# Kernel optimization log

Measured on AMD Instinct MI355X. Metric: run time of the kernel, lower is better.

## Reference

```python
import jax, jax.numpy as jnp
import numpy as np

ROBOT_W = 1.0
PHASE_W = 1.0
COHER_W = 10.0
SPEED_W = 5.0
MAX_SPEED = 10.0
SMOOTH_VEL_W = 0.05
SMOOTH_ACC_W = 0.01

# illegal phase transitions {(0,2),(1,0),(2,0),(2,1)} as a 3x3 lookup table
_ILLEGAL = np.zeros((3, 3), dtype=bool)
for a, b in [(0, 2), (1, 0), (2, 0), (2, 1)]:
    _ILLEGAL[a, b] = True
ILLEGAL_TABLE = jnp.asarray(_ILLEGAL)


def setup_inputs() -> dict:
    key = jax.random.key(0)
    k1, k2, k3, k4 = jax.random.split(key, 4)
    B, T = 256, 8192
    # scale by 8 so per-frame speeds (norm of diffs of 3-vectors) exceed MAX_SPEED
    pred_robot = jax.random.normal(k1, (B, T, 12), dtype=jnp.float32) * 8.0
    gt_robot = jax.random.normal(k2, (B, T, 12), dtype=jnp.float32) * 8.0
    pred_phase = jax.random.normal(k3, (B, T, 3), dtype=jnp.float32)
    gt_phase = jax.random.randint(k4, (B, T), 0, 3, dtype=jnp.int32)
    return {"pred_robot": pred_robot, "pred_phase": pred_phase,
            "gt_robot": gt_robot, "gt_phase": gt_phase}


def _coherence_loss(phase_logits):
    # vectorized replacement for the O(B*T) Python double loop
    p = jnp.argmax(phase_logits, axis=-1)            # [B, T]
    pt, pt1 = p[:, :-1], p[:, 1:]                    # [B, T-1]
    illegal = ILLEGAL_TABLE[pt, pt1]                 # [B, T-1] bool
    # logit of the (illegal) predicted phase at t+1
    sel = jnp.take_along_axis(phase_logits[:, 1:], pt1[..., None], axis=-1)[..., 0]
    loss_sum = jnp.sum(jnp.where(illegal, sel * sel, 0.0))
    count = jnp.sum(illegal)
    return jnp.where(count > 0, loss_sum / jnp.maximum(count, 1).astype(sel.dtype), 0.0)


def _speed_loss(pred_robot):
    B, T, D = pred_robot.shape
    vel = pred_robot[:, 1:] - pred_robot[:, :-1]     # [B, T-1, 12]
    pts = vel.reshape(B, T - 1, 4, 3)
    speeds = jnp.linalg.norm(pts, axis=-1)           # [B, T-1, 4]
    pen = jax.nn.relu(speeds - MAX_SPEED)
    return SPEED_W * jnp.mean(pen * pen)


def reference(pred_robot, pred_phase, gt_robot, gt_phase):
    # MSE over robot trajectory
    robot_loss = jnp.mean((pred_robot - gt_robot) ** 2)
    # cross-entropy over 3 phase classes
    logp = jax.nn.log_softmax(pred_phase, axis=-1)   # [B, T, 3]
    nll = -jnp.take_along_axis(logp, gt_phase[..., None].astype(jnp.int32), axis=-1)[..., 0]
    phase_loss = jnp.mean(nll)
    coherence = _coherence_loss(pred_phase)
    speed_loss = _speed_loss(pred_robot)
    vel = pred_robot[:, 1:] - pred_robot[:, :-1]
    vel_loss = jnp.mean(vel * vel)
    acc = pred_robot[:, 2:] - 2.0 * pred_robot[:, 1:-1] + pred_robot[:, :-2]
    acc_loss = jnp.mean(acc * acc)
    total = (ROBOT_W * robot_loss + PHASE_W * phase_loss + COHER_W * coherence
             + speed_loss + SMOOTH_VEL_W * vel_loss + SMOOTH_ACC_W * acc_loss)
    return total
```

## Files before the change

kernel.cpp:

```cpp
#include <hip/hip_runtime.h>
#include <math.h>

#define B_DIM 256
#define T_DIM 8192
#define BLOCK 256
#define GRID  1024
#define NSLOT 256
#define ROWS_TOT (B_DIM * T_DIM)
#define NPAIR (ROWS_TOT / 2)
#define NT    (GRID * BLOCK)
#define NITER (NPAIR / NT)
#define NF4   (ROWS_TOT * 3)


__device__ __forceinline__ float pen_term(float s) {
    float d = fmaxf(sqrtf(s) - 10.0f, 0.0f);
    return d * d;
}
__device__ __forceinline__ void argmax3(float l0, float l1, float l2, int &p, float &m) {
    p = 0; m = l0;
    if (l1 > m) { m = l1; p = 1; }
    if (l2 > m) { m = l2; p = 2; }
}
__device__ __forceinline__ float nll3(float l0, float l1, float l2, int g) {
    float mx = fmaxf(l0, fmaxf(l1, l2));
    float s = __expf(l0 - mx) + __expf(l1 - mx) + __expf(l2 - mx);
    float sel = (g == 0) ? l0 : ((g == 1) ? l1 : l2);
    return mx + __logf(s) - sel;
}
__device__ __forceinline__ void sse4(const float4 &a, const float4 &g, float &s) {
    float d;
    d = a.x - g.x; s = fmaf(d, d, s);  d = a.y - g.y; s = fmaf(d, d, s);
    d = a.z - g.z; s = fmaf(d, d, s);  d = a.w - g.w; s = fmaf(d, d, s);
}
__device__ __forceinline__ void vel12(const float4 &p0a, const float4 &p0b, const float4 &p0c,
                                      const float4 &p1a, const float4 &p1b, const float4 &p1c,
                                      float &velsq, float &pen2) {
    float t;
    t = p1a.x - p0a.x; const float q0  = t * t;
    t = p1a.y - p0a.y; const float q1  = t * t;
    t = p1a.z - p0a.z; const float q2  = t * t;
    t = p1a.w - p0a.w; const float q3  = t * t;
    t = p1b.x - p0b.x; const float q4  = t * t;
    t = p1b.y - p0b.y; const float q5  = t * t;
    t = p1b.z - p0b.z; const float q6  = t * t;
    t = p1b.w - p0b.w; const float q7  = t * t;
    t = p1c.x - p0c.x; const float q8  = t * t;
    t = p1c.y - p0c.y; const float q9  = t * t;
    t = p1c.z - p0c.z; const float q10 = t * t;
    t = p1c.w - p0c.w; const float q11 = t * t;
    velsq += (q0 + q1 + q2 + q3) + (q4 + q5 + q6 + q7) + (q8 + q9 + q10 + q11);
    pen2  += pen_term(q0 + q1 + q2) + pen_term(q3 + q4 + q5)
           + pen_term(q6 + q7 + q8) + pen_term(q9 + q10 + q11);
}
__device__ __forceinline__ void acc4(const float4 &r0, const float4 &r1, const float4 &r2, float &accsq) {
    float a;
    a = r2.x - 2.0f * r1.x + r0.x; accsq = fmaf(a, a, accsq);
    a = r2.y - 2.0f * r1.y + r0.y; accsq = fmaf(a, a, accsq);
    a = r2.z - 2.0f * r1.z + r0.z; accsq = fmaf(a, a, accsq);
    a = r2.w - 2.0f * r1.w + r0.w; accsq = fmaf(a, a, accsq);
}

__global__ __launch_bounds__(BLOCK, 4) void combined_loss_main(
    const float4* __restrict__ pred4,
    const float*  __restrict__ ph,
    const float4* __restrict__ gt4,
    const int*    __restrict__ gt_phase,
    double* __restrict__ ws)
{
    __shared__ float s_red[4][6];
    const int tid  = threadIdx.x;
    const int blk  = blockIdx.x;
    const int gtid = blk * BLOCK + tid;

    float sse = 0.f, nllv = 0.f, csum = 0.f, ccnt = 0.f;
    float pen2 = 0.f, velsq = 0.f, accsq = 0.f;

    #pragma unroll 1
    for (int u = 0; u < NITER; ++u) {
        const int P = u * NT + gtid;
        const bool tail = ((P + 1) & 4095) == 0;
        const size_t fp = (size_t)P * 6;
        const size_t ep = tail ? fp : fp + 6;

        const float4 A0 = pred4[fp + 0], A1 = pred4[fp + 1], A2 = pred4[fp + 2];
        const float4 A3 = pred4[fp + 3], A4 = pred4[fp + 4], A5 = pred4[fp + 5];
        const float4 G0 = gt4[fp + 0],   G1 = gt4[fp + 1],   G2 = gt4[fp + 2];
        const float4 G3 = gt4[fp + 3],   G4 = gt4[fp + 4],   G5 = gt4[fp + 5];
        const float4 E0 = pred4[ep + 0], E1 = pred4[ep + 1], E2 = pred4[ep + 2];
        const float4 E3 = pred4[ep + 3], E4 = pred4[ep + 4], E5 = pred4[ep + 5];

        sse4(A0, G0, sse); sse4(A1, G1, sse); sse4(A2, G2, sse);
        sse4(A3, G3, sse); sse4(A4, G4, sse); sse4(A5, G5, sse);

        vel12(A0, A1, A2, A3, A4, A5, velsq, pen2);
        if (!tail) {
            vel12(A3, A4, A5, E0, E1, E2, velsq, pen2);
            acc4(A0, A3, E0, accsq);
            acc4(A1, A4, E1, accsq);
            acc4(A2, A5, E2, accsq);
            acc4(A3, E0, E3, accsq);
            acc4(A4, E1, E4, accsq);
            acc4(A5, E2, E5, accsq);
        }
    }

    const float2* ph2  = (const float2*)ph;
    const int2*   gtp2 = (const int2*)gt_phase;
    #pragma unroll 1
    for (int u = 0; u < NITER; ++u) {
        const int L = u * NT + gtid;
        const bool tail = ((L + 1) & 4095) == 0;
        const size_t pb = (size_t)L * 3;
        const size_t qb = tail ? pb : pb + 3;

        const float2 a  = ph2[pb + 0], b = ph2[pb + 1], c = ph2[pb + 2];
        const float2 e0 = ph2[qb + 0], e1 = ph2[qb + 1];
        const int2   gg = gtp2[L];

        nllv += nll3(a.x, a.y, b.x, gg.x);
        nllv += nll3(b.y, c.x, c.y, gg.y);

        int p0, p1, p2; float m0, m1, m2;
        argmax3(a.x,  a.y,  b.x,  p0, m0);
        argmax3(b.y,  c.x,  c.y,  p1, m1);
        argmax3(e0.x, e0.y, e1.x, p2, m2);

        const int mask0 = (p0 == 0) ? 4 : ((p0 == 1) ? 1 : 3);
        if ((mask0 >> p1) & 1) { csum += m1 * m1; ccnt += 1.f; }
        if (!tail) {
            const int mask1 = (p1 == 0) ? 4 : ((p1 == 1) ? 1 : 3);
            if ((mask1 >> p2) & 1) { csum += m2 * m2; ccnt += 1.f; }
        }
    }

    float vals[6] = { fmaf(12.0f, nllv, sse), csum, ccnt, pen2, velsq, accsq };
    #pragma unroll
    for (int off = 32; off > 0; off >>= 1) {
        #pragma unroll
        for (int q = 0; q < 6; ++q)
            vals[q] += __shfl_down(vals[q], off, 64);
    }
    const int wave = tid >> 6, lane = tid & 63;
    if (lane == 0) {
        #pragma unroll
        for (int q = 0; q < 6; ++q) s_red[wave][q] = vals[q];
    }
    __syncthreads();
    if (tid < 6) {
        const double acc = (double)s_red[0][tid] + (double)s_red[1][tid]
                         + (double)s_red[2][tid] + (double)s_red[3][tid];
        atomicAdd(&ws[(size_t)(blk & (NSLOT - 1)) * 8 + tid], acc);
    }
}

__global__ __launch_bounds__(256) void combined_loss_final(
    const double* __restrict__ ws, float* __restrict__ out)
{
    __shared__ double sred[4][6];
    const int tid = threadIdx.x;
    double v[6];
    #pragma unroll
    for (int q = 0; q < 6; ++q) v[q] = ws[(size_t)tid * 8 + q];
    #pragma unroll
    for (int off = 32; off > 0; off >>= 1) {
        #pragma unroll
        for (int q = 0; q < 6; ++q)
            v[q] += __shfl_down(v[q], off, 64);
    }
    const int wave = tid >> 6, lane = tid & 63;
    if (lane == 0) {
        #pragma unroll
        for (int q = 0; q < 6; ++q) sred[wave][q] = v[q];
    }
    __syncthreads();
    if (tid == 0) {
        double s[6];
        #pragma unroll
        for (int q = 0; q < 6; ++q)
            s[q] = sred[0][q] + sred[1][q] + sred[2][q] + sred[3][q];
        const double robot_phase = s[0] / (double)((size_t)B_DIM * T_DIM * 12);
        const double coher = (s[2] > 0.0) ? (s[1] / fmax(s[2], 1.0)) : 0.0;
        const double speed = 5.0  * (s[3] / (double)((size_t)B_DIM * (T_DIM - 1) * 4));
        const double vel   = 0.05 * (s[4] / (double)((size_t)B_DIM * (T_DIM - 1) * 12));
        const double acc   = 0.01 * (s[5] / (double)((size_t)B_DIM * (T_DIM - 2) * 12));
        out[0] = (float)(robot_phase + 10.0 * coher + speed + vel + acc);
    }
}

extern "C" void kernel_launch(void* const* d_in, const int* in_sizes, int n_in,
                              void* d_out, int out_size, void* d_ws, size_t ws_size,
                              hipStream_t stream)
{
    const float4* pred4      = (const float4*)d_in[0];
    const float*  pred_phase = (const float*)d_in[1];
    const float4* gt4        = (const float4*)d_in[2];
    const int*    gt_phase   = (const int*)d_in[3];
    double* ws  = (double*)d_ws;
    float*  out = (float*)d_out;

    hipMemsetAsync(d_ws, 0, (size_t)NSLOT * 8 * sizeof(double), stream);

    combined_loss_main<<<dim3(GRID), BLOCK, 0, stream>>>(pred4, pred_phase, gt4, gt_phase, ws);
    combined_loss_final<<<1, 256, 0, stream>>>(ws, out);
}
```

Before: 243.5 us.

## Stage row tiles into double-buffered LDS via async global-to-LDS loads

```diff
diff --git a/kernel.cpp b/kernel.cpp
--- a/kernel.cpp
+++ b/kernel.cpp
@@ -4,14 +4,66 @@
 #define B_DIM 256
 #define T_DIM 8192
 #define BLOCK 256
-#define GRID  1024
 #define NSLOT 256
 #define ROWS_TOT (B_DIM * T_DIM)
-#define NPAIR (ROWS_TOT / 2)
-#define NT    (GRID * BLOCK)
-#define NITER (NPAIR / NT)
-#define NF4   (ROWS_TOT * 3)
-
+#define NF4  (ROWS_TOT * 3)
+#define TILE_ROWS 256
+#define NTILES (ROWS_TOT / TILE_ROWS)
+#define GRID 1024
+#define TPB (NTILES / GRID)
+
+#define L_GT   768
+#define L_PHG  1536
+#define BUF_F4 1792
+
+
+__device__ __forceinline__ void dma16(const void* g, void* l) {
+    __builtin_amdgcn_global_load_lds(
+        (const __attribute__((address_space(1))) void*)g,
+        (__attribute__((address_space(3))) void*)l, 16, 0, 0);
+}
+
+__device__ __forceinline__ void stage_tile(int R, int tid, float4* buf,
+    const float4* __restrict__ pred4, const float4* __restrict__ gt4,
+    const float*  __restrict__ ph,    const int*    __restrict__ gtp)
+{
+    const char* gp = (const char*)(pred4 + (size_t)R * 3);
+    const char* gg = (const char*)(gt4   + (size_t)R * 3);
+    char* lb = (char*)buf;
+    const int o = tid * 16;
+    dma16(gp + o,        lb + o);
+    dma16(gp + 4096 + o, lb + 4096 + o);
+    dma16(gp + 8192 + o, lb + 8192 + o);
+    dma16(gg + o,        lb + 12288 + o);
+    dma16(gg + 4096 + o, lb + 16384 + o);
+    dma16(gg + 8192 + o, lb + 20480 + o);
+    const char* gm = (tid < 192)
+        ? ((const char*)(ph + (size_t)R * 3) + o)
+        : ((const char*)(gtp + R) + (o - 3072));
+    dma16(gm, lb + 24576 + o);
+}
+
+struct Bnd {
+    float4 e0a, e0b, e0c;
+    float4 e1a, e1b, e1c;
+    float  q0, q1, q2;
+};
+
+__device__ __forceinline__ void load_bnd(int R, int tid, Bnd &b,
+    const float4* __restrict__ pred4, const float* __restrict__ ph)
+{
+    if (tid >= BLOCK - 2) {
+        int r1 = R + 256, r2 = R + 257;
+        if (r1 >= ROWS_TOT) r1 = R;
+        if (r2 >= ROWS_TOT) r2 = R;
+        const float4* p1 = pred4 + (size_t)r1 * 3;
+        const float4* p2 = pred4 + (size_t)r2 * 3;
+        b.e0a = p1[0]; b.e0b = p1[1]; b.e0c = p1[2];
+        b.e1a = p2[0]; b.e1b = p2[1]; b.e1c = p2[2];
+        const float* pp = ph + (size_t)r1 * 3;
+        b.q0 = pp[0]; b.q1 = pp[1]; b.q2 = pp[2];
+    }
+}
 
 __device__ __forceinline__ float pen_term(float s) {
     float d = fmaxf(sqrtf(s) - 10.0f, 0.0f);
@@ -61,77 +113,94 @@
     a = r2.w - 2.0f * r1.w + r0.w; accsq = fmaf(a, a, accsq);
 }
 
-__global__ __launch_bounds__(BLOCK, 4) void combined_loss_main(
+__global__ __launch_bounds__(BLOCK) void combined_loss_main(
     const float4* __restrict__ pred4,
     const float*  __restrict__ ph,
     const float4* __restrict__ gt4,
     const int*    __restrict__ gt_phase,
     double* __restrict__ ws)
 {
-    __shared__ float s_red[4][6];
-    const int tid  = threadIdx.x;
-    const int blk  = blockIdx.x;
-    const int gtid = blk * BLOCK + tid;
+    __shared__ float4 lds[2][BUF_F4];
+    __shared__ float  s_red[4][6];
+
+    const int tid = threadIdx.x;
+    const int blk = blockIdx.x;
+    const int t0  = blk * TPB;
 
     float sse = 0.f, nllv = 0.f, csum = 0.f, ccnt = 0.f;
     float pen2 = 0.f, velsq = 0.f, accsq = 0.f;
 
-    #pragma unroll 1
-    for (int u = 0; u < NITER; ++u) {
-        const int P = u * NT + gtid;
-        const bool tail = ((P + 1) & 4095) == 0;
-        const size_t fp = (size_t)P * 6;
-        const size_t ep = tail ? fp : fp + 6;
-
-        const float4 A0 = pred4[fp + 0], A1 = pred4[fp + 1], A2 = pred4[fp + 2];
-        const float4 A3 = pred4[fp + 3], A4 = pred4[fp + 4], A5 = pred4[fp + 5];
-        const float4 G0 = gt4[fp + 0],   G1 = gt4[fp + 1],   G2 = gt4[fp + 2];
-        const float4 G3 = gt4[fp + 3],   G4 = gt4[fp + 4],   G5 = gt4[fp + 5];
-        const float4 E0 = pred4[ep + 0], E1 = pred4[ep + 1], E2 = pred4[ep + 2];
-        const float4 E3 = pred4[ep + 3], E4 = pred4[ep + 4], E5 = pred4[ep + 5];
-
-        sse4(A0, G0, sse); sse4(A1, G1, sse); sse4(A2, G2, sse);
-        sse4(A3, G3, sse); sse4(A4, G4, sse); sse4(A5, G5, sse);
-
-        vel12(A0, A1, A2, A3, A4, A5, velsq, pen2);
-        if (!tail) {
-            vel12(A3, A4, A5, E0, E1, E2, velsq, pen2);
-            acc4(A0, A3, E0, accsq);
-            acc4(A1, A4, E1, accsq);
-            acc4(A2, A5, E2, accsq);
-            acc4(A3, E0, E3, accsq);
-            acc4(A4, E1, E4, accsq);
-            acc4(A5, E2, E5, accsq);
+    Bnd bA, bB;
+    load_bnd(t0 * TILE_ROWS, tid, bA, pred4, ph);
+    stage_tile(t0 * TILE_ROWS, tid, lds[0], pred4, gt4, ph, gt_phase);
+
+    for (int it = 0; it < TPB; ++it) {
+        const int R = (t0 + it) * TILE_ROWS;
+        float4* buf = lds[it & 1];
+
+        if (it + 1 < TPB) {
+            const int Rn = (t0 + it + 1) * TILE_ROWS;
+            load_bnd(Rn, tid, bB, pred4, ph);
+            stage_tile(Rn, tid, lds[(it + 1) & 1], pred4, gt4, ph, gt_phase);
+            asm volatile("s_waitcnt vmcnt(7)" ::: "memory");
+        } else {
+            asm volatile("s_waitcnt vmcnt(0)" ::: "memory");
         }
-    }
-
-    const float2* ph2  = (const float2*)ph;
-    const int2*   gtp2 = (const int2*)gt_phase;
-    #pragma unroll 1
-    for (int u = 0; u < NITER; ++u) {
-        const int L = u * NT + gtid;
-        const bool tail = ((L + 1) & 4095) == 0;
-        const size_t pb = (size_t)L * 3;
-        const size_t qb = tail ? pb : pb + 3;
-
-        const float2 a  = ph2[pb + 0], b = ph2[pb + 1], c = ph2[pb + 2];
-        const float2 e0 = ph2[qb + 0], e1 = ph2[qb + 1];
-        const int2   gg = gtp2[L];
-
-        nllv += nll3(a.x, a.y, b.x, gg.x);
-        nllv += nll3(b.y, c.x, c.y, gg.y);
-
-        int p0, p1, p2; float m0, m1, m2;
-        argmax3(a.x,  a.y,  b.x,  p0, m0);
-        argmax3(b.y,  c.x,  c.y,  p1, m1);
-        argmax3(e0.x, e0.y, e1.x, p2, m2);
-
-        const int mask0 = (p0 == 0) ? 4 : ((p0 == 1) ? 1 : 3);
-        if ((mask0 >> p1) & 1) { csum += m1 * m1; ccnt += 1.f; }
-        if (!tail) {
-            const int mask1 = (p1 == 0) ? 4 : ((p1 == 1) ? 1 : 3);
-            if ((mask1 >> p2) & 1) { csum += m2 * m2; ccnt += 1.f; }
+        asm volatile("s_barrier" ::: "memory");
+
+        {
+            const int row_g = R + tid;
+            const int t  = row_g & (T_DIM - 1);
+            const bool v1 = t < (T_DIM - 1);
+            const bool v2 = t < (T_DIM - 2);
+
+            const float4* sp = buf;
+            const float4* sg = buf + L_GT;
+            const float*  sf = (const float*)(buf + L_PHG);
+            const int*    sgt = (const int*)(sf + 768);
+            const int b3 = 3 * tid;
+
+            const float4 r0a = sp[b3], r0b = sp[b3 + 1], r0c = sp[b3 + 2];
+            const float4 g0a = sg[b3], g0b = sg[b3 + 1], g0c = sg[b3 + 2];
+
+            float4 r1a, r1b, r1c, r2a, r2b, r2c;
+            if (tid < BLOCK - 2) {
+                r1a = sp[b3 + 3]; r1b = sp[b3 + 4]; r1c = sp[b3 + 5];
+                r2a = sp[b3 + 6]; r2b = sp[b3 + 7]; r2c = sp[b3 + 8];
+            } else if (tid == BLOCK - 2) {
+                r1a = sp[b3 + 3]; r1b = sp[b3 + 4]; r1c = sp[b3 + 5];
+                r2a = bA.e0a;     r2b = bA.e0b;     r2c = bA.e0c;
+            } else {
+                r1a = bA.e0a;     r1b = bA.e0b;     r1c = bA.e0c;
+                r2a = bA.e1a;     r2b = bA.e1b;     r2c = bA.e1c;
+            }
+
+            sse4(r0a, g0a, sse); sse4(r0b, g0b, sse); sse4(r0c, g0c, sse);
+            if (v1) vel12(r0a, r0b, r0c, r1a, r1b, r1c, velsq, pen2);
+            if (v2) {
+                acc4(r0a, r1a, r2a, accsq);
+                acc4(r0b, r1b, r2b, accsq);
+                acc4(r0c, r1c, r2c, accsq);
+            }
+
+            const float p00 = sf[b3], p01 = sf[b3 + 1], p02 = sf[b3 + 2];
+            float p10, p11, p12;
+            if (tid < BLOCK - 1) { p10 = sf[b3 + 3]; p11 = sf[b3 + 4]; p12 = sf[b3 + 5]; }
+            else                 { p10 = bA.q0;      p11 = bA.q1;      p12 = bA.q2; }
+
+            nllv += nll3(p00, p01, p02, sgt[tid]);
+            if (v1) {
+                int pP, pN; float mP, mN;
+                argmax3(p00, p01, p02, pP, mP);
+                argmax3(p10, p11, p12, pN, mN);
+                const int mask = (pP == 0) ? 4 : ((pP == 1) ? 1 : 3);
+                if ((mask >> pN) & 1) { csum += mN * mN; ccnt += 1.f; }
+            }
         }
+
+        asm volatile("s_waitcnt lgkmcnt(0)" ::: "memory");
+        asm volatile("s_barrier" ::: "memory");
+        bA = bB;
     }
 
     float vals[6] = { fmaf(12.0f, nllv, sse), csum, ccnt, pen2, velsq, accsq };
```

Result: no change. 244.5 us (+0.4%).
